# Optimization experiments

Hardware: AMD Instinct MI355X
Metric: run time of the kernel (lower is better)

The kernel has to match this reference:

```python
import jax, jax.numpy as jnp
import numpy as np

WH, WW = 8, 8
N = WH * WW
DIM = 128
NUM_HEADS = 4
HEAD_DIM = DIM // NUM_HEADS
SCALE = HEAD_DIM ** -0.5


def _relative_position_index():
    coords = np.stack(np.meshgrid(np.arange(WH), np.arange(WW), indexing='ij'))  # (2, Wh, Ww)
    flat = coords.reshape(2, -1)  # (2, N)
    rel = flat[:, :, None] - flat[:, None, :]  # (2, N, N)
    rel = rel.transpose(1, 2, 0)  # (N, N, 2)
    rel[:, :, 0] += WH - 1
    rel[:, :, 1] += WW - 1
    rel[:, :, 0] *= 2 * WW - 1
    return rel.sum(-1)  # (N, N) int

REL_IDX = _relative_position_index()


def setup_inputs() -> dict:
    key = jax.random.key(0)
    ks = jax.random.split(key, 7)
    B_ = 4096
    nW = 64
    table_size = (2 * WH - 1) * (2 * WW - 1)  # 225
    return {
        'x': jax.random.normal(ks[0], (B_, N, DIM), dtype=jnp.float32),
        'mask': jax.random.normal(ks[1], (nW, N, N), dtype=jnp.float32),
        'qkv_w': jax.random.normal(ks[2], (3 * DIM, DIM), dtype=jnp.float32) * 0.02,
        'qkv_b': jnp.zeros((3 * DIM,), dtype=jnp.float32),
        'proj_w': jax.random.normal(ks[3], (DIM, DIM), dtype=jnp.float32) * 0.02,
        'proj_b': jnp.zeros((DIM,), dtype=jnp.float32),
        'bias_table': jax.random.normal(ks[4], (table_size, NUM_HEADS), dtype=jnp.float32) * 0.02,
    }


def reference(x, mask, qkv_w, qkv_b, proj_w, proj_b, bias_table):
    B_, n, C = x.shape
    nW = mask.shape[0]
    qkv = x @ qkv_w.T + qkv_b  # (B_, N, 3C)
    qkv = qkv.reshape(B_, n, 3, NUM_HEADS, HEAD_DIM)
    q = qkv[:, :, 0] * SCALE  # (B_, N, H, hd)
    k = qkv[:, :, 1]
    v = qkv[:, :, 2]
    attn = jnp.einsum('bihd,bjhd->bhij', q, k)  # (B_, H, N, N)
    rel_bias = bias_table[REL_IDX.reshape(-1)].reshape(n, n, NUM_HEADS)
    attn = attn + rel_bias.transpose(2, 0, 1)[None]  # broadcast over B_
    attn = attn.reshape(B_ // nW, nW, NUM_HEADS, n, n) + mask[None, :, None]
    attn = attn.reshape(B_, NUM_HEADS, n, n)
    attn = jax.nn.softmax(attn, axis=-1)
    out = jnp.einsum('bhij,bjhd->bihd', attn, v).reshape(B_, n, C)
    return out @ proj_w.T + proj_b
```

## Files before the change

kernel.cpp:

```cpp
#include <hip/hip_runtime.h>


typedef __bf16 bf16x8 __attribute__((ext_vector_type(8)));
typedef float f32x16 __attribute__((ext_vector_type(16)));

#define MFMA32(a, b, c) __builtin_amdgcn_mfma_f32_32x32x16_bf16(a, b, c, 0, 0, 0)
#define ATT_SCALE 0.17677669529663687f

__device__ __forceinline__ unsigned short f2bf(float f) {
  union { float fv; unsigned int u; } cv; cv.fv = f;
  unsigned int r = cv.u + 0x7FFFu + ((cv.u >> 16) & 1u);
  return (unsigned short)(r >> 16);
}

__device__ __forceinline__ unsigned pk2(float lo, float hi) {
  union { __bf16 h[2]; unsigned u; } t;
  t.h[0] = (__bf16)lo; t.h[1] = (__bf16)hi;
  return t.u;
}

__device__ __forceinline__ void pairw(float l0, float l1, float h0, float h1,
                                      int hl, unsigned &wlo, unsigned &whi) {
  unsigned lo = pk2(l0, l1);
  unsigned hi = pk2(h0, h1);
  unsigned los = (unsigned)__shfl_xor((int)lo, 32);
  unsigned his = (unsigned)__shfl_xor((int)hi, 32);
  wlo = hl ? his : lo;
  whi = hl ? hi : los;
}

__device__ __forceinline__ bf16x8 frag8(float a0, float a1, float a2, float a3,
                                        float a4, float a5, float a6, float a7,
                                        int hl) {
  union { unsigned u[4]; bf16x8 v; } r;
  pairw(a0, a1, a4, a5, hl, r.u[0], r.u[2]);
  pairw(a2, a3, a6, a7, hl, r.u[1], r.u[3]);
  return r.v;
}

#define FRAG_LO(p) frag8(p[0], p[1], p[2], p[3], p[4], p[5], p[6], p[7], hl)
#define FRAG_HI(p) frag8(p[8], p[9], p[10], p[11], p[12], p[13], p[14], p[15], hl)

__global__ __launch_bounds__(256) void prep(
    const float* __restrict__ mask, const float* __restrict__ bias_table,
    const float* __restrict__ qkv_w, const float* __restrict__ proj_w,
    float* __restrict__ maskT, float* __restrict__ relT,
    unsigned short* __restrict__ wq, unsigned short* __restrict__ wp) {
  const int blk = blockIdx.x;
  const int tid = threadIdx.x;
  if (blk < 64) {
    __shared__ float T[64][65];
    const float* mp = mask + (size_t)blk * 4096;
    #pragma unroll
    for (int rr = 0; rr < 16; ++rr) {
      int e = rr * 256 + tid;
      T[e >> 6][e & 63] = mp[e];
    }
    __syncthreads();
    float* op = maskT + (size_t)blk * 4096;
    #pragma unroll
    for (int rr = 0; rr < 16; ++rr) {
      int e = rr * 256 + tid;
      op[e] = T[e & 63][e >> 6];
    }
  } else if (blk < 80) {
    int t0 = (blk - 64) * 256 + tid;
    #pragma unroll
    for (int u = 0; u < 4; ++u) {
      int t = u * 4096 + t0;
      int ji = t & 4095;
      int h = t >> 12;
      int j = ji >> 6, i = ji & 63;
      int ridx = ((i >> 3) - (j >> 3) + 7) * 15 + ((i & 7) - (j & 7) + 7);
      relT[t] = bias_table[ridx * 4 + h];
    }
  } else {
    int t = ((blk - 80) * 256 + tid) * 4;
    if (t < 49152) {
      float4 v = *reinterpret_cast<const float4*>(qkv_w + t);
      float sc = (t < 16384) ? ATT_SCALE : 1.0f;
      ushort4 o;
      o.x = f2bf(v.x * sc); o.y = f2bf(v.y * sc);
      o.z = f2bf(v.z * sc); o.w = f2bf(v.w * sc);
      *reinterpret_cast<ushort4*>(wq + t) = o;
    } else {
      int tp = t - 49152;
      float4 v = *reinterpret_cast<const float4*>(proj_w + tp);
      ushort4 o;
      o.x = f2bf(v.x); o.y = f2bf(v.y); o.z = f2bf(v.z); o.w = f2bf(v.w);
      *reinterpret_cast<ushort4*>(wp + tp) = o;
    }
  }
}

__global__ __launch_bounds__(256, 3) void window_attn(
    const float* __restrict__ x, const float* __restrict__ qkv_b,
    const float* __restrict__ proj_b, const unsigned short* __restrict__ wq,
    const unsigned short* __restrict__ wp, const float* __restrict__ maskT,
    const float* __restrict__ relT, float* __restrict__ out, int nW) {
  __shared__ unsigned short Xb[64][136];
  __shared__ unsigned short Vt[4][32][72];
  __shared__ unsigned short Ob[64][136];

  const int tid = threadIdx.x;
  const int h = tid >> 6;
  const int lane = tid & 63;
  const int l31 = lane & 31;
  const int hl = lane >> 5;
  const int b = blockIdx.x;
  const int w = b % nW;

  const float* xb = x + (size_t)b * 8192;
  #pragma unroll
  for (int st = 0; st < 8; ++st) {
    int e = (st * 256 + tid) * 4;
    float4 v4 = *reinterpret_cast<const float4*>(xb + e);
    ushort4 o;
    o.x = f2bf(v4.x); o.y = f2bf(v4.y); o.z = f2bf(v4.z); o.w = f2bf(v4.w);
    *reinterpret_cast<ushort4*>(&Xb[e >> 7][e & 127]) = o;
  }
  __syncthreads();

  {
    f32x16 av0, av1;
    #pragma unroll
    for (int q = 0; q < 16; ++q) { av0[q] = 0.0f; av1[q] = 0.0f; }
    const unsigned short* wvp = wq + (size_t)(256 + h * 32 + l31) * 128 + hl * 8;
    #pragma unroll
    for (int kt = 0; kt < 8; ++kt) {
      bf16x8 aw = *reinterpret_cast<const bf16x8*>(wvp + kt * 16);
      bf16x8 b0 = *reinterpret_cast<const bf16x8*>(&Xb[l31][kt * 16 + hl * 8]);
      bf16x8 b1 = *reinterpret_cast<const bf16x8*>(&Xb[32 + l31][kt * 16 + hl * 8]);
      av0 = MFMA32(aw, b0, av0);
      av1 = MFMA32(aw, b1, av1);
    }
    #pragma unroll
    for (int r = 0; r < 16; ++r) {
      int dr = (r & 3) + 8 * (r >> 2) + 4 * hl;
      float bv = qkv_b[256 + h * 32 + dr];
      Vt[h][dr][l31]      = f2bf(av0[r] + bv);
      Vt[h][dr][32 + l31] = f2bf(av1[r] + bv);
    }
  }

  bf16x8 qf[2][2], kf[2][2];
  {
    f32x16 aq[2], ak[2];
    #pragma unroll
    for (int t2 = 0; t2 < 2; ++t2)
      #pragma unroll
      for (int q = 0; q < 16; ++q) { aq[t2][q] = 0.0f; ak[t2][q] = 0.0f; }
    const unsigned short* wqp = wq + (size_t)(h * 32 + l31) * 128 + hl * 8;
    const unsigned short* wkp = wq + (size_t)(128 + h * 32 + l31) * 128 + hl * 8;
    #pragma unroll
    for (int kt = 0; kt < 8; ++kt) {
      bf16x8 b0 = *reinterpret_cast<const bf16x8*>(&Xb[l31][kt * 16 + hl * 8]);
      bf16x8 b1 = *reinterpret_cast<const bf16x8*>(&Xb[32 + l31][kt * 16 + hl * 8]);
      bf16x8 awq = *reinterpret_cast<const bf16x8*>(wqp + kt * 16);
      bf16x8 awk = *reinterpret_cast<const bf16x8*>(wkp + kt * 16);
      aq[0] = MFMA32(awq, b0, aq[0]);
      aq[1] = MFMA32(awq, b1, aq[1]);
      ak[0] = MFMA32(awk, b0, ak[0]);
      ak[1] = MFMA32(awk, b1, ak[1]);
    }

    #pragma unroll
    for (int r = 0; r < 16; ++r) {
      int dr = (r & 3) + 8 * (r >> 2) + 4 * hl;
      float bq = qkv_b[h * 32 + dr] * ATT_SCALE;
      float bk = qkv_b[128 + h * 32 + dr];
      aq[0][r] += bq; aq[1][r] += bq;
      ak[0][r] += bk; ak[1][r] += bk;
    }

    #pragma unroll
    for (int t2 = 0; t2 < 2; ++t2) {
      kf[t2][0] = FRAG_LO(ak[t2]); kf[t2][1] = FRAG_HI(ak[t2]);
    }
    #pragma unroll
    for (int t2 = 0; t2 < 2; ++t2) {
      qf[t2][0] = FRAG_LO(aq[t2]); qf[t2][1] = FRAG_HI(aq[t2]);
    }
  }

  const float* mkp = maskT + ((size_t)w << 12);
  const float* rlp = relT + ((size_t)h << 12);
  #pragma unroll
  for (int it = 0; it < 2; ++it) {
    f32x16 s[2];
    #pragma unroll
    for (int mt = 0; mt < 2; ++mt)
      #pragma unroll
      for (int r = 0; r < 16; ++r) {
        int off = ((r & 3) + 8 * (r >> 2) + 4 * hl + 32 * mt) * 64 + 32 * it + l31;
        s[mt][r] = mkp[off] + rlp[off];
      }
    #pragma unroll
    for (int mt = 0; mt < 2; ++mt) {
      s[mt] = MFMA32(kf[mt][0], qf[it][0], s[mt]);
      s[mt] = MFMA32(kf[mt][1], qf[it][1], s[mt]);
    }

    float mx[8];
    #pragma unroll
    for (int r = 0; r < 8; ++r)
      mx[r] = fmaxf(fmaxf(s[0][r], s[0][r + 8]), fmaxf(s[1][r], s[1][r + 8]));
    mx[0] = fmaxf(mx[0], mx[4]); mx[1] = fmaxf(mx[1], mx[5]);
    mx[2] = fmaxf(mx[2], mx[6]); mx[3] = fmaxf(mx[3], mx[7]);
    float m = fmaxf(fmaxf(mx[0], mx[1]), fmaxf(mx[2], mx[3]));
    m = fmaxf(m, __shfl_xor(m, 32));
    #pragma unroll
    for (int mt = 0; mt < 2; ++mt)
      #pragma unroll
      for (int r = 0; r < 16; ++r)
        s[mt][r] = __expf(s[mt][r] - m);
    float sm[8];
    #pragma unroll
    for (int r = 0; r < 8; ++r)
      sm[r] = (s[0][r] + s[0][r + 8]) + (s[1][r] + s[1][r + 8]);
    sm[0] += sm[4]; sm[1] += sm[5]; sm[2] += sm[6]; sm[3] += sm[7];
    float sum = (sm[0] + sm[1]) + (sm[2] + sm[3]);
    sum += __shfl_xor(sum, 32);
    const float rinv = __builtin_amdgcn_rcpf(sum);

    bf16x8 pf[4];
    pf[0] = FRAG_LO(s[0]); pf[1] = FRAG_HI(s[0]);
    pf[2] = FRAG_LO(s[1]); pf[3] = FRAG_HI(s[1]);

    f32x16 o;
    #pragma unroll
    for (int q = 0; q < 16; ++q) o[q] = 0.0f;
    #pragma unroll
    for (int kt = 0; kt < 4; ++kt) {
      bf16x8 aV = *reinterpret_cast<const bf16x8*>(&Vt[h][l31][kt * 16 + hl * 8]);
      o = MFMA32(aV, pf[kt], o);
    }
    #pragma unroll
    for (int r = 0; r < 16; ++r) {
      int dr = (r & 3) + 8 * (r >> 2) + 4 * hl;
      Ob[32 * it + l31][h * 32 + dr] = f2bf(o[r] * rinv);
    }
  }
  __syncthreads();

  {
    const int c = h * 32 + l31;
    const float pb = proj_b[c];
    const unsigned short* wrow = wp + (size_t)c * 128 + hl * 8;
    bf16x8 bfr[8];
    #pragma unroll
    for (int kt = 0; kt < 8; ++kt)
      bfr[kt] = *reinterpret_cast<const bf16x8*>(wrow + kt * 16);
    float* ob = out + (size_t)b * 8192;
    #pragma unroll
    for (int mt = 0; mt < 2; ++mt) {
      f32x16 acc;
      #pragma unroll
      for (int q = 0; q < 16; ++q) acc[q] = 0.0f;
      #pragma unroll
      for (int kt = 0; kt < 8; ++kt) {
        bf16x8 a = *reinterpret_cast<const bf16x8*>(&Ob[mt * 32 + l31][kt * 16 + hl * 8]);
        acc = MFMA32(a, bfr[kt], acc);
      }
      #pragma unroll
      for (int r = 0; r < 16; ++r) {
        int row = (r & 3) + 8 * (r >> 2) + 4 * hl + mt * 32;
        ob[row * 128 + c] = acc[r] + pb;
      }
    }
  }
}

extern "C" void kernel_launch(void* const* d_in, const int* in_sizes, int n_in,
                              void* d_out, int out_size, void* d_ws, size_t ws_size,
                              hipStream_t stream) {
  const float* x          = (const float*)d_in[0];
  const float* mask       = (const float*)d_in[1];
  const float* qkv_w      = (const float*)d_in[2];
  const float* qkv_b      = (const float*)d_in[3];
  const float* proj_w     = (const float*)d_in[4];
  const float* proj_b     = (const float*)d_in[5];
  const float* bias_table = (const float*)d_in[6];
  const int B_ = in_sizes[0] / 8192;
  const int nW = in_sizes[1] / 4096;

  unsigned short* wq = (unsigned short*)d_ws;
  unsigned short* wp = wq + 384 * 128;
  float* maskT = (float*)((char*)d_ws + 131072);
  float* relT  = (float*)((char*)d_ws + 131072 + (size_t)nW * 4096 * 4);

  prep<<<144, 256, 0, stream>>>(mask, bias_table, qkv_w, proj_w, maskT, relT, wq, wp);
  window_attn<<<B_, 256, 0, stream>>>(x, qkv_b, proj_b, wq, wp, maskT, relT, (float*)d_out, nW);
}
```

Measured before the change: 302.5 us.

## Reuse X shared buffer for attention output and fold log2e into exp2 softmax

Drops the separate Ob shared-memory buffer and writes the attention output into the Xb buffer, with an extra barrier after the Q/K projection so no wave overwrites Xb while others still read it. The smaller shared footprint allows raising launch bounds from 3 to 4 blocks per CU. The log2(e) factor is folded into the mask, the relative bias and the Q weights and bias, so the softmax can use exp2f directly. Manual float-to-bf16 rounding is replaced with native __bf16 casts and packed conversions. The tighter register budget may cause spills, and the added barrier adds a synchronisation point.

```diff
diff --git a/kernel.cpp b/kernel.cpp
--- a/kernel.cpp
+++ b/kernel.cpp
@@ -6,11 +6,13 @@
 
 #define MFMA32(a, b, c) __builtin_amdgcn_mfma_f32_32x32x16_bf16(a, b, c, 0, 0, 0)
 #define ATT_SCALE 0.17677669529663687f
-
-__device__ __forceinline__ unsigned short f2bf(float f) {
-  union { float fv; unsigned int u; } cv; cv.fv = f;
-  unsigned int r = cv.u + 0x7FFFu + ((cv.u >> 16) & 1u);
-  return (unsigned short)(r >> 16);
+#define LOG2E     1.4426950408889634f
+#define QSCL      (ATT_SCALE * LOG2E)
+
+__device__ __forceinline__ unsigned short bfu(float f) {
+  union { __bf16 b; unsigned short u; } c;
+  c.b = (__bf16)f;
+  return c.u;
 }
 
 __device__ __forceinline__ unsigned pk2(float lo, float hi) {
@@ -61,7 +63,7 @@
     #pragma unroll
     for (int rr = 0; rr < 16; ++rr) {
       int e = rr * 256 + tid;
-      op[e] = T[e & 63][e >> 6];
+      op[e] = T[e & 63][e >> 6] * LOG2E;
     }
   } else if (blk < 80) {
     int t0 = (blk - 64) * 256 + tid;
@@ -72,35 +74,35 @@
       int h = t >> 12;
       int j = ji >> 6, i = ji & 63;
       int ridx = ((i >> 3) - (j >> 3) + 7) * 15 + ((i & 7) - (j & 7) + 7);
-      relT[t] = bias_table[ridx * 4 + h];
+      relT[t] = bias_table[ridx * 4 + h] * LOG2E;
     }
   } else {
     int t = ((blk - 80) * 256 + tid) * 4;
     if (t < 49152) {
       float4 v = *reinterpret_cast<const float4*>(qkv_w + t);
-      float sc = (t < 16384) ? ATT_SCALE : 1.0f;
-      ushort4 o;
-      o.x = f2bf(v.x * sc); o.y = f2bf(v.y * sc);
-      o.z = f2bf(v.z * sc); o.w = f2bf(v.w * sc);
-      *reinterpret_cast<ushort4*>(wq + t) = o;
+      float sc = (t < 16384) ? QSCL : 1.0f;
+      uint2 o;
+      o.x = pk2(v.x * sc, v.y * sc);
+      o.y = pk2(v.z * sc, v.w * sc);
+      *reinterpret_cast<uint2*>(wq + t) = o;
     } else {
       int tp = t - 49152;
       float4 v = *reinterpret_cast<const float4*>(proj_w + tp);
-      ushort4 o;
-      o.x = f2bf(v.x); o.y = f2bf(v.y); o.z = f2bf(v.z); o.w = f2bf(v.w);
-      *reinterpret_cast<ushort4*>(wp + tp) = o;
-    }
-  }
-}
-
-__global__ __launch_bounds__(256, 3) void window_attn(
+      uint2 o;
+      o.x = pk2(v.x, v.y);
+      o.y = pk2(v.z, v.w);
+      *reinterpret_cast<uint2*>(wp + tp) = o;
+    }
+  }
+}
+
+__global__ __launch_bounds__(256, 4) void window_attn(
     const float* __restrict__ x, const float* __restrict__ qkv_b,
     const float* __restrict__ proj_b, const unsigned short* __restrict__ wq,
     const unsigned short* __restrict__ wp, const float* __restrict__ maskT,
     const float* __restrict__ relT, float* __restrict__ out, int nW) {
   __shared__ unsigned short Xb[64][136];
   __shared__ unsigned short Vt[4][32][72];
-  __shared__ unsigned short Ob[64][136];
 
   const int tid = threadIdx.x;
   const int h = tid >> 6;
@@ -115,9 +117,10 @@
   for (int st = 0; st < 8; ++st) {
     int e = (st * 256 + tid) * 4;
     float4 v4 = *reinterpret_cast<const float4*>(xb + e);
-    ushort4 o;
-    o.x = f2bf(v4.x); o.y = f2bf(v4.y); o.z = f2bf(v4.z); o.w = f2bf(v4.w);
-    *reinterpret_cast<ushort4*>(&Xb[e >> 7][e & 127]) = o;
+    uint2 o;
+    o.x = pk2(v4.x, v4.y);
+    o.y = pk2(v4.z, v4.w);
+    *reinterpret_cast<uint2*>(&Xb[e >> 7][e & 127]) = o;
   }
   __syncthreads();
 
@@ -138,8 +141,8 @@
     for (int r = 0; r < 16; ++r) {
       int dr = (r & 3) + 8 * (r >> 2) + 4 * hl;
       float bv = qkv_b[256 + h * 32 + dr];
-      Vt[h][dr][l31]      = f2bf(av0[r] + bv);
-      Vt[h][dr][32 + l31] = f2bf(av1[r] + bv);
+      Vt[h][dr][l31]      = bfu(av0[r] + bv);
+      Vt[h][dr][32 + l31] = bfu(av1[r] + bv);
     }
   }
 
@@ -163,11 +166,12 @@
       ak[0] = MFMA32(awk, b0, ak[0]);
       ak[1] = MFMA32(awk, b1, ak[1]);
     }
+    __syncthreads();
 
     #pragma unroll
     for (int r = 0; r < 16; ++r) {
       int dr = (r & 3) + 8 * (r >> 2) + 4 * hl;
-      float bq = qkv_b[h * 32 + dr] * ATT_SCALE;
+      float bq = qkv_b[h * 32 + dr] * QSCL;
       float bk = qkv_b[128 + h * 32 + dr];
       aq[0][r] += bq; aq[1][r] += bq;
       ak[0][r] += bk; ak[1][r] += bk;
@@ -213,7 +217,7 @@
     for (int mt = 0; mt < 2; ++mt)
       #pragma unroll
       for (int r = 0; r < 16; ++r)
-        s[mt][r] = __expf(s[mt][r] - m);
+        s[mt][r] = exp2f(s[mt][r] - m);
     float sm[8];
     #pragma unroll
     for (int r = 0; r < 8; ++r)
@@ -238,7 +242,7 @@
     #pragma unroll
     for (int r = 0; r < 16; ++r) {
       int dr = (r & 3) + 8 * (r >> 2) + 4 * hl;
-      Ob[32 * it + l31][h * 32 + dr] = f2bf(o[r] * rinv);
+      Xb[32 * it + l31][h * 32 + dr] = bfu(o[r] * rinv);
     }
   }
   __syncthreads();
@@ -259,7 +263,7 @@
       for (int q = 0; q < 16; ++q) acc[q] = 0.0f;
       #pragma unroll
       for (int kt = 0; kt < 8; ++kt) {
-        bf16x8 a = *reinterpret_cast<const bf16x8*>(&Ob[mt * 32 + l31][kt * 16 + hl * 8]);
+        bf16x8 a = *reinterpret_cast<const bf16x8*>(&Xb[mt * 32 + l31][kt * 16 + hl * 8]);
         acc = MFMA32(a, bfr[kt], acc);
       }
       #pragma unroll
```

After: 324.8 us. +7.4%, slower.
